# Kernel optimization log

Measured on AMD Instinct MI355X. Metric: run time of the kernel, lower is better.

The kernel has to match this reference:

```python
import jax, jax.numpy as jnp
import numpy as np

# ---- module configuration (mirrors __init__ args) ----
NT, NX = 200, 256          # len(T), len(X)
EPS = 1.0
T_GRID = np.linspace(0.0, 1.0, NT)
X_GRID = np.linspace(0.0, 1.0, NX)
DT = float(T_GRID[1] - T_GRID[0])
DX = float(X_GRID[1] - X_GRID[0])

# graph converted to index form (as __init__ does with keys.index):
# node -> {parent_index: power}. Nodes 0 (xi/dW) and 1 (u_0/I_c) are sources.
GRAPH = [{}, {}, {0: 1}, {1: 1}, {0: 2}, {0: 1, 1: 1}, {2: 2},
         {2: 1, 1: 1}, {2: 3}, {0: 1, 2: 1}, {1: 2}, {4: 1, 2: 1}]


def parabolic_matrix(N, dt, dx, BC, eps=EPS):
    """Transposed inverse implicit-Euler heat matrix, as in Parabolic_Matrix(...).T"""
    A = np.diag(-2.0 * np.ones(N + 1)) + np.diag(np.ones(N), 1) + np.diag(np.ones(N), -1)
    if BC == 'D':
        A[0, 0] = A[0, 1] = A[1, 0] = 0.0
        A[-1, -1] = A[-1, -2] = A[-2, -1] = 0.0
    if BC == 'N':
        A[0, 1] = 2.0
        A[-1, -2] = 2.0
    if BC == 'P':
        A[-1, 1] = 1.0
        A[0, -2] = 1.0
    return np.linalg.inv(np.eye(N + 1) - eps * dt * A / dx ** 2).T


M = jnp.asarray(parabolic_matrix(NX - 1, DT, DX, 'P'), jnp.float32)    # self.M
M_C = jnp.asarray(parabolic_matrix(NX - 1, DT, DX, 'D'), jnp.float32)  # self.M_c


def setup_inputs() -> dict:
    key = jax.random.key(0)
    k1, k2 = jax.random.split(key)
    W = jax.random.normal(k1, (128, NT, NX), dtype=jnp.float32)
    U0 = jax.random.normal(k2, (128, NX), dtype=jnp.float32)
    return {"W": W, "U0": U0}


def reference(W, U0):
    # dW[:,0]=0 ; dW[:,1:]=diff(W,axis=1)/dt   (diff=True branch)
    dW = jnp.concatenate([jnp.zeros_like(W[:, :1]), jnp.diff(W, axis=1) / DT], axis=1)

    # I_c(U0): Solution[:,i] = Solution[:,i-1] @ M_c, Solution[:,0]=U0
    def ic_step(y, _):
        y = y @ M_C
        return y, y
    _, sol = jax.lax.scan(ic_step, U0, None, length=NT - 1)          # [NT-1,B,NX]
    ic = jnp.concatenate([U0[:, None, :], jnp.moveaxis(sol, 0, 1)], axis=1)  # [B,NT,NX]

    feats = [dW, ic]

    def int_step(y, t):
        y = (y + t * DT) @ M
        return y, y

    for dic in GRAPH[2:]:
        # tmp = prod over parents of feats[it]**p  (parents are earlier nodes)
        tmp = jnp.ones_like(dW)
        for it, p in dic.items():
            tmp = tmp * (feats[it] if p == 1 else feats[it] ** p)
        # integrated[:,i,:,k] = (integrated[:,i-1,:,k] + tmp[:,i,:]*dt) @ M, i=1..NT-1
        xs = jnp.moveaxis(tmp[:, 1:, :], 1, 0)                       # [NT-1,B,NX]
        _, ys = jax.lax.scan(int_step, jnp.zeros_like(U0), xs)       # [NT-1,B,NX]
        feats.append(jnp.concatenate([jnp.zeros_like(U0)[:, None, :],
                                      jnp.moveaxis(ys, 0, 1)], axis=1))

    return jnp.stack(feats, axis=-1)  # [B, NT, NX, n_graph]
```

## Files before the change

kernel.cpp:

```cpp
#include <hip/hip_runtime.h>

#define IDTF 199.0f
#define DTF  (1.0f/199.0f)
#define RING 12

typedef float f4 __attribute__((ext_vector_type(4)));

__device__ __forceinline__ void lds_barrier() {
    asm volatile("s_waitcnt lgkmcnt(0)\n\ts_barrier" ::: "memory");
}
__device__ __forceinline__ float bp(int idx, float v) {
    return __builtin_bit_cast(float,
        __builtin_amdgcn_ds_bpermute(idx, __builtin_bit_cast(int, v)));
}

__global__ void k_pcr(float* __restrict__ C) {
    const double cc = 65025.0 / 199.0;
    __shared__ double pa[2][256], pb[2][256], pc[2][256];
    __shared__ double AL[8][256], BE[8][256];
    __shared__ double ca[256], cb[256], ccx[256];
    __shared__ double salp0[64], sbet0[64];
    __shared__ double Ah[64], Bh[64], Ch[64];
    __shared__ double AL6[6][64], BE6[6][64];
    const int x = threadIdx.x;

    {
        double ai = (x == 0) ? 0.0 : -cc;
        double bi = 1.0 + 2.0 * cc;
        double ci = (x == 255) ? 0.0 : -cc;
        int cur = 0;
        pa[0][x] = ai; pb[0][x] = bi; pc[0][x] = ci;
        __syncthreads();
        for (int l = 0; l < 8; l++) {
            int s = 1 << l, xm = (x - s < 0) ? 0 : x - s, xp = (x + s > 255) ? 255 : x + s;
            double al = pa[cur][x] / pb[cur][xm];
            double be = pc[cur][x] / pb[cur][xp];
            AL[l][x] = al; BE[l][x] = be;
            double an = -al * pa[cur][xm];
            double cn = -be * pc[cur][xp];
            double bn = pb[cur][x] - al * pc[cur][xm] - be * pa[cur][xp];
            pa[1 - cur][x] = an; pb[1 - cur][x] = bn; pc[1 - cur][x] = cn;
            __syncthreads();
            cur ^= 1;
        }
        double invd = 1.0 / pb[cur][x];
        __syncthreads();
        int cw = 0;
        pa[0][x] = (x == 0) ? -cc : 0.0;
        pc[0][x] = (x == 255) ? -cc : 0.0;
        __syncthreads();
        for (int l = 0; l < 8; l++) {
            int s = 1 << l, xm = (x - s < 0) ? 0 : x - s, xp = (x + s > 255) ? 255 : x + s;
            double n1 = pa[cw][x] - AL[l][x] * pa[cw][xm] - BE[l][x] * pa[cw][xp];
            double n2 = pc[cw][x] - AL[l][x] * pc[cw][xm] - BE[l][x] * pc[cw][xp];
            pa[1 - cw][x] = n1; pc[1 - cw][x] = n2;
            __syncthreads();
            cw ^= 1;
        }
        double t1 = pa[cw][x] * invd, t2 = pc[cw][x] * invd;
        pa[1 - cw][x] = t1; pc[1 - cw][x] = t2;
        __syncthreads();
        double K00 = 1.0 + pa[1 - cw][254], K01 = pc[1 - cw][254];
        double K10 = pa[1 - cw][1],         K11 = 1.0 + pc[1 - cw][1];
        double idet = 1.0 / (K00 * K11 - K01 * K10);
        C[5120 + x] = (float)(t1 * (K11 * idet) + t2 * (-K10 * idet));
        C[5376 + x] = (float)(t1 * (-K01 * idet) + t2 * (K00 * idet));
        __syncthreads();
    }
    for (int m = 0; m < 2; m++) {
        double ai, bi, ci;
        if (m == 0) {
            ai = (x == 0) ? 0.0 : -cc;
            bi = 1.0 + 2.0 * cc;
            ci = (x == 255) ? 0.0 : -cc;
        } else {
            if (x == 0 || x == 255) { ai = 0.0; bi = 1.0; ci = 0.0; }
            else {
                ai = (x == 1) ? 0.0 : -cc;
                bi = 1.0 + 2.0 * cc;
                ci = (x == 254) ? 0.0 : -cc;
            }
        }
        ca[x] = ai; cb[x] = bi; ccx[x] = ci;
        __syncthreads();
        float* Cr = C + m * 2560;
        double as_ = 0, cs_ = 0, bs_ = 0, alp2 = 0, bet2 = 0;
        if (x < 64) {
            int r0 = 4 * x;
            double m00 = cb[r0],     m01 = ccx[r0];
            double m10 = ca[r0 + 1], m11 = cb[r0 + 1], m12 = ccx[r0 + 1];
            double m21 = ca[r0 + 2], m22 = cb[r0 + 2];
            double C00 = m11 * m22 - m12 * m21, C01 = -m10 * m22, C02 = m10 * m21;
            double C10 = -m01 * m22, C11 = m00 * m22, C12 = -m00 * m21;
            double C20 = m01 * m12, C21 = -m00 * m12, C22 = m00 * m11 - m01 * m10;
            double det = m00 * C00 + m01 * C01;
            double id = 1.0 / det;
            double Mi[3][3] = {{C00 * id, C10 * id, C20 * id},
                               {C01 * id, C11 * id, C21 * id},
                               {C02 * id, C12 * id, C22 * id}};
            double aL = ca[r0], cR = ccx[r0 + 2];
            double alp[3], bet[3];
            for (int i = 0; i < 3; i++) { alp[i] = Mi[i][0] * aL; bet[i] = Mi[i][2] * cR; }
            salp0[x] = alp[0]; sbet0[x] = bet[0];
            as_ = ca[r0 + 3]; cs_ = ccx[r0 + 3]; bs_ = cb[r0 + 3];
            alp2 = alp[2]; bet2 = bet[2];
            for (int i = 0; i < 3; i++)
                for (int j = 0; j < 3; j++)
                    Cr[(i * 3 + j) * 64 + x] = (float)Mi[i][j];
            for (int i = 0; i < 3; i++) {
                Cr[(9 + i) * 64 + x] = (float)alp[i];
                Cr[(12 + i) * 64 + x] = (float)bet[i];
            }
            Cr[15 * 64 + x] = (float)as_;
            Cr[16 * 64 + x] = (float)cs_;
        }
        __syncthreads();
        if (x < 64) {
            int xp = (x + 1) & 63;
            double a0n = salp0[xp], b0n = sbet0[xp];
            Ah[x] = -as_ * alp2;
            Bh[x] = bs_ - as_ * bet2 - cs_ * a0n;
            Ch[x] = -cs_ * b0n;
        }
        __syncthreads();
        double bfin = 1.0;
        for (int l = 0; l < 6; l++) {
            int s = 1 << l;
            double an = 0, bn = 1, cn = 0;
            if (x < 64) {
                double Acur = Ah[x], Bcur = Bh[x], Ccur = Ch[x];
                double Am = (x - s >= 0) ? Ah[x - s] : 0.0;
                double Bm = (x - s >= 0) ? Bh[x - s] : 1.0;
                double Cm = (x - s >= 0) ? Ch[x - s] : 0.0;
                double Ap = (x + s < 64) ? Ah[x + s] : 0.0;
                double Bp = (x + s < 64) ? Bh[x + s] : 1.0;
                double Cp = (x + s < 64) ? Ch[x + s] : 0.0;
                double al = (x - s >= 0) ? Acur / Bm : 0.0;
                double be = (x + s < 64) ? Ccur / Bp : 0.0;
                AL6[l][x] = al; BE6[l][x] = be;
                an = -al * Am;
                cn = -be * Cp;
                bn = Bcur - al * Cm - be * Ap;
            }
            __syncthreads();
            if (x < 64) { Ah[x] = an; Bh[x] = bn; Ch[x] = cn; bfin = bn; }
            __syncthreads();
        }
        if (x < 64) {
            for (int p = 0; p < 3; p++) {
                int s2 = 2 * (1 << (2 * p));
                double a0 = AL6[2 * p][x],     b0 = BE6[2 * p][x];
                double a1 = AL6[2 * p + 1][x], b1 = BE6[2 * p + 1][x];
                double am = (x - s2 >= 0) ? AL6[2 * p][x - s2] : 0.0;
                double bm = (x - s2 >= 0) ? BE6[2 * p][x - s2] : 0.0;
                double ap = (x + s2 < 64) ? AL6[2 * p][x + s2] : 0.0;
                double bq = (x + s2 < 64) ? BE6[2 * p][x + s2] : 0.0;
                Cr[(17 + p * 6 + 0) * 64 + x] = (float)(-a1 * am);
                Cr[(17 + p * 6 + 1) * 64 + x] = (float)(a1);
                Cr[(17 + p * 6 + 2) * 64 + x] = (float)(a0 - a1 * bm);
                Cr[(17 + p * 6 + 3) * 64 + x] = (float)(b0 - b1 * ap);
                Cr[(17 + p * 6 + 4) * 64 + x] = (float)(b1);
                Cr[(17 + p * 6 + 5) * 64 + x] = (float)(-b1 * bq);
            }
            Cr[35 * 64 + x] = (float)(1.0 / bfin);
        }
        __syncthreads();
    }
}

__global__ __launch_bounds__(512, 1) void k_split(const float* __restrict__ W,
        const float* __restrict__ U0, const float* __restrict__ C,
        float* __restrict__ out) {
    const int bid = blockIdx.x;
    const int role = (bid >> 3) & 1;
    const int b = (bid & 7) | ((bid >> 4) << 3);
    const int tid = threadIdx.x;
    const int wv = tid >> 6;
    const int L = tid & 63;

    static const signed char TY[8]      = {0,1,2,3,3,3,3,4};
    static const signed char FMT[2][8]  = {{0,0,0,4,1,3,2,0},{0,0,0,0,1,3,2,0}};
    static const signed char PAT[2][8]  = {{0,0,0,1,1,0,2,0},{0,0,0,0,0,1,1,0}};
    static const signed char PBT[2][8]  = {{0,0,0,0,0,0,1,0},{0,0,0,0,0,0,0,0}};
    static const signed char PUB[2][8]  = {{0,1,2,3,4,5,6,0},{0,1,4,3,5,6,7,0}};
    static const signed char NW[8]      = {0,1,1,0,1,0,0,0};
    static const signed char WGRP[2][2]    = {{2,-1},{0,1}};
    static const signed char WPL[2][2][4]  = {{{3,4,5,6},{0,0,0,0}},
                                              {{2,0,1,3},{4,5,6,7}}};

    const int  ty    = TY[wv];
    const bool isWr  = (ty == 4);
    const bool isIC  = (ty == 0);
    const bool isProd = (ty <= 2);
    const int  fmode = FMT[role][wv];
    const int  pAi = PAT[role][wv], pBi = PBT[role][wv];
    const int  pubP  = PUB[role][wv];
    const bool needW = NW[wv];
    const bool pubDW = (role == 1 && wv == 1);
    const int  mat   = isIC ? 1 : 0;

    const float* Cr = C + mat * 2560;
    float fMi[9], nalp[3], nbet[3], nst[3][6];
#pragma unroll
    for (int k = 0; k < 9; k++) fMi[k] = Cr[k * 64 + L];
#pragma unroll
    for (int i = 0; i < 3; i++) {
        nalp[i] = -Cr[(9 + i) * 64 + L];
        nbet[i] = -Cr[(12 + i) * 64 + L];
    }
    const float nas = -Cr[15 * 64 + L];
    const float ncs = -Cr[16 * 64 + L];
#pragma unroll
    for (int p = 0; p < 3; p++)
#pragma unroll
        for (int k = 0; k < 6; k++) nst[p][k] = -Cr[(17 + p * 6 + k) * 64 + L];
    const float invdX = Cr[35 * 64 + L];
    float npk0[4], npk1[4];
    {
        f4 p0 = *(const f4*)&C[5120 + 4 * L];
        f4 p1 = *(const f4*)&C[5376 + 4 * L];
#pragma unroll
        for (int q = 0; q < 4; q++) { npk0[q] = -p0[q]; npk1[q] = -p1[q]; }
    }
    int ixm[3][3], ixp[3][3];
#pragma unroll
    for (int p = 0; p < 3; p++) {
        const int sg = (p == 0) ? 1 : ((p == 1) ? 4 : 16);
#pragma unroll
        for (int k = 0; k < 3; k++) {
            ixm[p][k] = ((L - (k + 1) * sg) & 63) << 2;
            ixp[p][k] = ((L + (k + 1) * sg) & 63) << 2;
        }
    }

    __shared__ f4 ring[RING][8][64];

    float y[4] = {0.f, 0.f, 0.f, 0.f};
    if (isIC) {
        f4 u0v = *(const f4*)&U0[b * 256 + 4 * L];
#pragma unroll
        for (int q = 0; q < 4; q++) y[q] = u0v[q];
    }
    if (isWr) {
        f4* of4 = (f4*)out;
        size_t rb = (size_t)b * 200 * 768;
#pragma unroll
        for (int g = 0; g < 2; g++) {
            const int wg = WGRP[role][g];
            if (wg < 0) continue;
#pragma unroll
            for (int q = 0; q < 4; q++) {
                int xx = 4 * L + q;
                f4 v = {0.f, 0.f, 0.f, 0.f};
                if (wg == 0) v[1] = U0[b * 256 + xx];
                of4[rb + (size_t)xx * 3 + wg] = v;
            }
        }
    }
    float wprev[4] = {0,0,0,0}, wcur[4] = {0,0,0,0}, wnxt[4] = {0,0,0,0};
    if (needW) {
        f4 w0 = *(const f4*)&W[((size_t)b * 200 + 0) * 256 + 4 * L];
        f4 w1 = *(const f4*)&W[((size_t)b * 200 + 1) * 256 + 4 * L];
#pragma unroll
        for (int q = 0; q < 4; q++) { wprev[q] = w0[q]; wcur[q] = w1[q]; }
    }
    __syncthreads();

    int slot = 1;
    int wslot = 1;

    for (int s = 0; s <= 51; s++) {
        if (!isWr) {
            for (int k = 1; k <= 4; k++) {
                const int j = 4 * s + k;
                const int t = isProd ? j : (j - 4);
                const bool active = isProd ? (j <= 199) : (j >= 5 && j <= 203);
                if (!active) continue;
                float dwv[4] = {0,0,0,0};
                if (needW) {
#pragma unroll
                    for (int q = 0; q < 4; q++) dwv[q] = (wcur[q] - wprev[q]) * IDTF;
                    if (t <= 198) {
                        f4 wn = *(const f4*)&W[((size_t)b * 200 + t + 1) * 256 + 4 * L];
#pragma unroll
                        for (int q = 0; q < 4; q++) wnxt[q] = wn[q];
                    }
                }
                float d[4];
                if (isProd) {
                    if (ty == 0) {
#pragma unroll
                        for (int q = 0; q < 4; q++) d[q] = y[q];
                    } else if (ty == 1) {
#pragma unroll
                        for (int q = 0; q < 4; q++) d[q] = fmaf(dwv[q], DTF, y[q]);
                    } else {
#pragma unroll
                        for (int q = 0; q < 4; q++) d[q] = fmaf(dwv[q] * dwv[q], DTF, y[q]);
                    }
                } else {
                    f4 pa = ring[slot][pAi][L];
                    f4 pb2 = (fmode == 2) ? ring[slot][pBi][L] : pa;
#pragma unroll
                    for (int q = 0; q < 4; q++) {
                        float fq;
                        if (fmode == 0)      fq = pa[q];
                        else if (fmode == 1) fq = dwv[q] * pa[q];
                        else if (fmode == 2) fq = pb2[q] * pa[q];
                        else if (fmode == 3) fq = pa[q] * pa[q];
                        else                 fq = pa[q] * pa[q] * pa[q];
                        d[q] = fmaf(fq, DTF, y[q]);
                    }
                }
                float u0 = fmaf(fMi[2], d[2], fmaf(fMi[1], d[1], fMi[0] * d[0]));
                float u1 = fmaf(fMi[5], d[2], fmaf(fMi[4], d[1], fMi[3] * d[0]));
                float u2 = fmaf(fMi[8], d[2], fmaf(fMi[7], d[1], fMi[6] * d[0]));
                float X = fmaf(nas, u2, fmaf(ncs, bp(ixp[0][0], u0), d[3]));
#pragma unroll
                for (int p = 0; p < 3; p++) {
                    float m3 = bp(ixm[p][2], X), m2 = bp(ixm[p][1], X), m1 = bp(ixm[p][0], X);
                    float q1 = bp(ixp[p][0], X), q2 = bp(ixp[p][1], X), q3 = bp(ixp[p][2], X);
                    float t0 = fmaf(nst[p][0], m3, fmaf(nst[p][1], m2, X));
                    float t1 = fmaf(nst[p][2], m1, fmaf(nst[p][3], q1, t0));
                    X = fmaf(nst[p][4], q2, fmaf(nst[p][5], q3, t1));
                }
                X *= invdX;
                float Xm = bp(ixm[0][0], X);
                d[0] = fmaf(nalp[0], Xm, fmaf(nbet[0], X, u0));
                d[1] = fmaf(nalp[1], Xm, fmaf(nbet[1], X, u1));
                d[2] = fmaf(nalp[2], Xm, fmaf(nbet[2], X, u2));
                d[3] = X;
                if (!isIC) {
                    float s1 = __builtin_bit_cast(float,
                        __builtin_amdgcn_readlane(__builtin_bit_cast(int, d[2]), 63));
                    float s2 = __builtin_bit_cast(float,
                        __builtin_amdgcn_readlane(__builtin_bit_cast(int, d[1]), 0));
#pragma unroll
                    for (int q = 0; q < 4; q++)
                        d[q] = fmaf(npk0[q], s1, fmaf(npk1[q], s2, d[q]));
                }
#pragma unroll
                for (int q = 0; q < 4; q++) y[q] = d[q];
                {
                    f4 pk; pk[0] = y[0]; pk[1] = y[1]; pk[2] = y[2]; pk[3] = y[3];
                    ring[slot][pubP][L] = pk;
                }
                if (pubDW) {
                    f4 pk; pk[0] = dwv[0]; pk[1] = dwv[1]; pk[2] = dwv[2]; pk[3] = dwv[3];
                    ring[slot][2][L] = pk;
                }
                if (needW && t <= 198) {
#pragma unroll
                    for (int q = 0; q < 4; q++) { wprev[q] = wcur[q]; wcur[q] = wnxt[q]; }
                }
                slot = (slot == RING - 1) ? 0 : (slot + 1);
            }
        } else {
            f4* of4 = (f4*)out;
#pragma unroll
            for (int k = 0; k < 4; k++) {
                const int tw = 4 * s - 7 + k;
                if (tw < 1 || tw > 199) continue;
                size_t rb = ((size_t)b * 200 + tw) * 768;
#pragma unroll
                for (int g = 0; g < 2; g++) {
                    const int wg = WGRP[role][g];
                    if (wg < 0) continue;
                    f4 p0 = ring[wslot][WPL[role][g][0]][L];
                    f4 p1 = ring[wslot][WPL[role][g][1]][L];
                    f4 p2 = ring[wslot][WPL[role][g][2]][L];
                    f4 p3 = ring[wslot][WPL[role][g][3]][L];
#pragma unroll
                    for (int q = 0; q < 4; q++) {
                        f4 v; v[0] = p0[q]; v[1] = p1[q]; v[2] = p2[q]; v[3] = p3[q];
                        of4[rb + (size_t)(4 * L + q) * 3 + wg] = v;
                    }
                }
                wslot = (wslot == RING - 1) ? 0 : (wslot + 1);
            }
        }
        lds_barrier();
    }
}

extern "C" void kernel_launch(void* const* d_in, const int* in_sizes, int n_in,
                              void* d_out, int out_size, void* d_ws, size_t ws_size,
                              hipStream_t stream) {
    const float* W = (const float*)d_in[0];
    const float* U0 = (const float*)d_in[1];
    float* out = (float*)d_out;
    float* C = (float*)d_ws;

    k_pcr<<<1, 256, 0, stream>>>(C);
    k_split<<<dim3(256), 512, 0, stream>>>(W, U0, C, out);
}
```

Baseline: 205.3 us.

## Fold first PCR stage into precomputed stencil and prefetch ring loads per step

Rewrites the first stride-1 reduction stage so the ncs*shift(u0) term is folded algebraically into a 7-point stencil with precomputed combined coefficients. That allows the 12 ds_bpermute calls on v and u0 to be issued in parallel instead of a serial bpermute followed by a dependent stage, shortening the per-timestep critical path. It also hoists the four ring-buffer LDS reads for a 4-step group to the start of the group, so their latency overlaps compute. The cost is more bpermutes per step and higher register pressure from the prefetched f4 values and extra coefficient arrays.

```diff
diff --git a/kernel.cpp b/kernel.cpp
--- a/kernel.cpp
+++ b/kernel.cpp
@@ -200,7 +200,7 @@
     const int  mat   = isIC ? 1 : 0;
 
     const float* Cr = C + mat * 2560;
-    float fMi[9], nalp[3], nbet[3], nst[3][6];
+    float fMi[9], nalp[3], nbet[3];
 #pragma unroll
     for (int k = 0; k < 9; k++) fMi[k] = Cr[k * 64 + L];
 #pragma unroll
@@ -209,12 +209,25 @@
         nbet[i] = -Cr[(12 + i) * 64 + L];
     }
     const float nas = -Cr[15 * 64 + L];
-    const float ncs = -Cr[16 * 64 + L];
-#pragma unroll
-    for (int p = 0; p < 3; p++)
-#pragma unroll
-        for (int k = 0; k < 6; k++) nst[p][k] = -Cr[(17 + p * 6 + k) * 64 + L];
+    float nst0v[6], nstA[6], nstB[6];
+#pragma unroll
+    for (int k = 0; k < 6; k++) {
+        nst0v[k] = -Cr[(17 + k) * 64 + L];
+        nstA[k]  = -Cr[(23 + k) * 64 + L];
+        nstB[k]  = -Cr[(29 + k) * 64 + L];
+    }
     const float invdX = Cr[35 * 64 + L];
+    float ncsm[7];
+#pragma unroll
+    for (int m = 0; m < 7; m++) ncsm[m] = -Cr[16 * 64 + ((L + m - 3) & 63)];
+    float gam[7];
+    gam[0] = nst0v[0] * ncsm[0];
+    gam[1] = nst0v[1] * ncsm[1];
+    gam[2] = nst0v[2] * ncsm[2];
+    gam[3] = ncsm[3];
+    gam[4] = nst0v[3] * ncsm[4];
+    gam[5] = nst0v[4] * ncsm[5];
+    gam[6] = nst0v[5] * ncsm[6];
     float npk0[4], npk1[4];
     {
         f4 p0 = *(const f4*)&C[5120 + 4 * L];
@@ -222,16 +235,19 @@
 #pragma unroll
         for (int q = 0; q < 4; q++) { npk0[q] = -p0[q]; npk1[q] = -p1[q]; }
     }
-    int ixm[3][3], ixp[3][3];
-#pragma unroll
-    for (int p = 0; p < 3; p++) {
-        const int sg = (p == 0) ? 1 : ((p == 1) ? 4 : 16);
-#pragma unroll
-        for (int k = 0; k < 3; k++) {
-            ixm[p][k] = ((L - (k + 1) * sg) & 63) << 2;
-            ixp[p][k] = ((L + (k + 1) * sg) & 63) << 2;
-        }
-    }
+    int ixv[6], ixu[6], ixs1[6], ixs2[6];
+    {
+        const int OV[6] = {-3,-2,-1,1,2,3};
+        const int OU[6] = {-2,-1,1,2,3,4};
+#pragma unroll
+        for (int k = 0; k < 6; k++) {
+            ixv[k] = ((L + OV[k]) & 63) << 2;
+            ixu[k] = ((L + OU[k]) & 63) << 2;
+            ixs1[k] = ((L + OV[k] * 4) & 63) << 2;
+            ixs2[k] = ((L + OV[k] * 16) & 63) << 2;
+        }
+    }
+    const int ixm1 = ((L + 63) & 63) << 2;
 
     __shared__ f4 ring[RING][8][64];
 
@@ -271,6 +287,20 @@
 
     for (int s = 0; s <= 51; s++) {
         if (!isWr) {
+            f4 paf[4], pbf[4];
+            if (!isProd) {
+                int sl = slot;
+#pragma unroll
+                for (int kk = 0; kk < 4; kk++) {
+                    const int jj = 4 * s + kk + 1;
+                    if (jj >= 5 && jj <= 203) {
+                        paf[kk] = ring[sl][pAi][L];
+                        pbf[kk] = (fmode == 2) ? ring[sl][pBi][L] : paf[kk];
+                        sl = (sl == RING - 1) ? 0 : (sl + 1);
+                    }
+                }
+            }
+#pragma unroll
             for (int k = 1; k <= 4; k++) {
                 const int j = 4 * s + k;
                 const int t = isProd ? j : (j - 4);
@@ -299,8 +329,8 @@
                         for (int q = 0; q < 4; q++) d[q] = fmaf(dwv[q] * dwv[q], DTF, y[q]);
                     }
                 } else {
-                    f4 pa = ring[slot][pAi][L];
-                    f4 pb2 = (fmode == 2) ? ring[slot][pBi][L] : pa;
+                    f4 pa = paf[k - 1];
+                    f4 pb2 = pbf[k - 1];
 #pragma unroll
                     for (int q = 0; q < 4; q++) {
                         float fq;
@@ -315,17 +345,34 @@
                 float u0 = fmaf(fMi[2], d[2], fmaf(fMi[1], d[1], fMi[0] * d[0]));
                 float u1 = fmaf(fMi[5], d[2], fmaf(fMi[4], d[1], fMi[3] * d[0]));
                 float u2 = fmaf(fMi[8], d[2], fmaf(fMi[7], d[1], fMi[6] * d[0]));
-                float X = fmaf(nas, u2, fmaf(ncs, bp(ixp[0][0], u0), d[3]));
-#pragma unroll
-                for (int p = 0; p < 3; p++) {
-                    float m3 = bp(ixm[p][2], X), m2 = bp(ixm[p][1], X), m1 = bp(ixm[p][0], X);
-                    float q1 = bp(ixp[p][0], X), q2 = bp(ixp[p][1], X), q3 = bp(ixp[p][2], X);
-                    float t0 = fmaf(nst[p][0], m3, fmaf(nst[p][1], m2, X));
-                    float t1 = fmaf(nst[p][2], m1, fmaf(nst[p][3], q1, t0));
-                    X = fmaf(nst[p][4], q2, fmaf(nst[p][5], q3, t1));
+                float v = fmaf(nas, u2, d[3]);
+                float va0 = bp(ixv[0], v), va1 = bp(ixv[1], v), va2 = bp(ixv[2], v);
+                float va3 = bp(ixv[3], v), va4 = bp(ixv[4], v), va5 = bp(ixv[5], v);
+                float ua0 = bp(ixu[0], u0), ua1 = bp(ixu[1], u0), ua2 = bp(ixu[2], u0);
+                float ua3 = bp(ixu[3], u0), ua4 = bp(ixu[4], u0), ua5 = bp(ixu[5], u0);
+                float X = fmaf(gam[2], u0, v);
+                X = fmaf(nst0v[0], va0, fmaf(nst0v[1], va1, X));
+                X = fmaf(nst0v[2], va2, fmaf(nst0v[3], va3, X));
+                X = fmaf(nst0v[4], va4, fmaf(nst0v[5], va5, X));
+                X = fmaf(gam[0], ua0, fmaf(gam[1], ua1, X));
+                X = fmaf(gam[3], ua2, fmaf(gam[4], ua3, X));
+                X = fmaf(gam[5], ua4, fmaf(gam[6], ua5, X));
+                {
+                    float m3 = bp(ixs1[0], X), m2 = bp(ixs1[1], X), m1 = bp(ixs1[2], X);
+                    float q1 = bp(ixs1[3], X), q2 = bp(ixs1[4], X), q3 = bp(ixs1[5], X);
+                    float t0 = fmaf(nstA[0], m3, fmaf(nstA[1], m2, X));
+                    float t1 = fmaf(nstA[2], m1, fmaf(nstA[3], q1, t0));
+                    X = fmaf(nstA[4], q2, fmaf(nstA[5], q3, t1));
+                }
+                {
+                    float m3 = bp(ixs2[0], X), m2 = bp(ixs2[1], X), m1 = bp(ixs2[2], X);
+                    float q1 = bp(ixs2[3], X), q2 = bp(ixs2[4], X), q3 = bp(ixs2[5], X);
+                    float t0 = fmaf(nstB[0], m3, fmaf(nstB[1], m2, X));
+                    float t1 = fmaf(nstB[2], m1, fmaf(nstB[3], q1, t0));
+                    X = fmaf(nstB[4], q2, fmaf(nstB[5], q3, t1));
                 }
                 X *= invdX;
-                float Xm = bp(ixm[0][0], X);
+                float Xm = bp(ixm1, X);
                 d[0] = fmaf(nalp[0], Xm, fmaf(nbet[0], X, u0));
                 d[1] = fmaf(nalp[1], Xm, fmaf(nbet[1], X, u1));
                 d[2] = fmaf(nalp[2], Xm, fmaf(nbet[2], X, u2));
```

Result: slower. 261.5 us (+27.4%).
